# Optimization experiments

Hardware: AMD Instinct MI355X
Metric: run time of the kernel (lower is better)

Reference implementation:

```python
import jax, jax.numpy as jnp
import numpy as np

C = 256
HEADS = 8
HD = C // HEADS
EPS = 1e-5


def _layernorm(x, g, b):
    mu = jnp.mean(x, axis=-1, keepdims=True)
    var = jnp.var(x, axis=-1, keepdims=True)
    return (x - mu) * jax.lax.rsqrt(var + EPS) * g + b


def setup_inputs() -> dict:
    key = jax.random.key(0)
    ks = jax.random.split(key, 16)
    s = 0.02
    return {
        "x": jax.random.normal(ks[0], (1, C, 64, 64), jnp.float32),
        "bn_gamma": 1.0 + s * jax.random.normal(ks[1], (C,), jnp.float32),
        "bn_beta": s * jax.random.normal(ks[2], (C,), jnp.float32),
        "bn_mean": s * jax.random.normal(ks[3], (C,), jnp.float32),
        "bn_var": jnp.ones((C,), jnp.float32),
        "w_in": s * jax.random.normal(ks[4], (C, C), jnp.float32),
        "b_in": jnp.zeros((C,), jnp.float32),
        "ln1_g": jnp.ones((C,), jnp.float32),
        "ln1_b": jnp.zeros((C,), jnp.float32),
        "w_qkv": s * jax.random.normal(ks[5], (3 * C, C), jnp.float32),
        "b_qkv": jnp.zeros((3 * C,), jnp.float32),
        "w_ap": s * jax.random.normal(ks[6], (C, C), jnp.float32),
        "b_ap": jnp.zeros((C,), jnp.float32),
        "ln2_g": jnp.ones((C,), jnp.float32),
        "ln2_b": jnp.zeros((C,), jnp.float32),
        "w_ff1": s * jax.random.normal(ks[7], (4 * C, C), jnp.float32),
        "b_ff1": jnp.zeros((4 * C,), jnp.float32),
        "w_ff2": s * jax.random.normal(ks[8], (C, 4 * C), jnp.float32),
        "b_ff2": jnp.zeros((C,), jnp.float32),
        "w_out": s * jax.random.normal(ks[9], (C, C), jnp.float32),
        "b_out": jnp.zeros((C,), jnp.float32),
    }


def reference(x, bn_gamma, bn_beta, bn_mean, bn_var, w_in, b_in,
              ln1_g, ln1_b, w_qkv, b_qkv, w_ap, b_ap,
              ln2_g, ln2_b, w_ff1, b_ff1, w_ff2, b_ff2, w_out, b_out):
    b, c, h, w = x.shape
    t = h * w
    x_in = x
    # BatchNorm2d (eval mode: running stats)
    xn = (x - bn_mean[None, :, None, None]) * jax.lax.rsqrt(bn_var + EPS)[None, :, None, None]
    xn = xn * bn_gamma[None, :, None, None] + bn_beta[None, :, None, None]
    # proj_in 1x1 conv -> tokens [b, t, c]
    tok = xn.reshape(b, c, t).transpose(0, 2, 1)
    tok = tok @ w_in.T + b_in
    # transformer block (depth=1)
    y = _layernorm(tok, ln1_g, ln1_b)  # norm1
    qkv = y @ w_qkv.T + b_qkv  # [b, t, 3c], channel split (3, H, hd)
    qkv = qkv.reshape(b, t, 3, HEADS, HD)
    q = qkv[:, :, 0].transpose(0, 2, 1, 3)  # [b, H, t, hd]
    k = qkv[:, :, 1].transpose(0, 2, 1, 3)
    v = qkv[:, :, 2].transpose(0, 2, 1, 3)
    scale = HD ** (-0.5)
    attn = jax.nn.softmax(jnp.einsum('bhqd,bhkd->bhqk', q, k) * scale, axis=-1)
    o = jnp.einsum('bhqk,bhkd->bhqd', attn, v)  # [b, H, t, hd]
    o = o.transpose(0, 2, 1, 3).reshape(b, t, c)  # channels ordered (H, hd)
    o = o @ w_ap.T + b_ap  # attn proj 1x1
    attn_out = o + y  # VanillaAttention residual adds its (normed) input
    tok = tok + attn_out
    # FFN
    z = _layernorm(tok, ln2_g, ln2_b)
    z = jax.nn.gelu(z @ w_ff1.T + b_ff1, approximate=False)
    tok = tok + (z @ w_ff2.T + b_ff2)
    # back to image, proj_out 1x1, outer residual
    x4 = tok.transpose(0, 2, 1).reshape(b, c, h, w)
    out = jnp.einsum('oc,bchw->bohw', w_out, x4) + b_out[None, :, None, None]
    return out + x_in
```

## Files before the change

kernel.cpp:

```cpp
#include <hip/hip_runtime.h>
#include <math.h>

#define T_TOK 4096
#define C_DIM 256
#define EPSF  1e-5f
#define SC_QL (0.17677669529663687f * 1.4426950408889634f)

typedef short  bf16x8  __attribute__((ext_vector_type(8)));
typedef float  f32x4   __attribute__((ext_vector_type(4)));
typedef ushort ushort8 __attribute__((ext_vector_type(8)));
typedef unsigned uint4v __attribute__((ext_vector_type(4)));

__device__ __forceinline__ short f2bf(float f) {
    unsigned u = __builtin_bit_cast(unsigned, f);
    unsigned r = (u + 0x7FFFu + ((u >> 16) & 1u)) >> 16;
    return (short)r;
}
__device__ __forceinline__ float bf2f(ushort u) {
    return __builtin_bit_cast(float, ((unsigned)u) << 16);
}
__device__ __forceinline__ unsigned pk_bf16(float a, float b) {
    const unsigned ua = __builtin_bit_cast(unsigned, a) + 0x8000u;
    const unsigned ub = __builtin_bit_cast(unsigned, b) + 0x8000u;
    return __builtin_amdgcn_perm(ub, ua, 0x07060302u);
}
__device__ __forceinline__ unsigned cvtpk_bf16(float a, float b) {
    unsigned r;
    asm("v_cvt_pk_bf16_f32 %0, %1, %2" : "=v"(r) : "v"(a), "v"(b));
    return r;
}
__device__ __forceinline__ void plswap32(unsigned &a, unsigned &b) {
    asm("v_permlane32_swap_b32 %0, %1" : "+v"(a), "+v"(b));
}
__device__ __forceinline__ void plswap16(unsigned &a, unsigned &b) {
    asm("v_permlane16_swap_b32 %0, %1" : "+v"(a), "+v"(b));
}
template <int CTRL>
__device__ __forceinline__ float dppf(float x) {
    return __builtin_bit_cast(float,
        __builtin_amdgcn_mov_dpp(__builtin_bit_cast(int, x), CTRL, 0xF, 0xF, true));
}
__device__ __forceinline__ float rowsum16(float x) {
    x += dppf<0xB1>(x);
    x += dppf<0x4E>(x);
    x += dppf<0x141>(x);
    x += dppf<0x140>(x);
    return x;
}
#define MFMA16(a, b, c) __builtin_amdgcn_mfma_f32_16x16x32_bf16(a, b, c, 0, 0, 0)

__global__ __launch_bounds__(256) void prep_kernel(
    const float* __restrict__ w_in, const float* __restrict__ w_qkv,
    const float* __restrict__ w_ap, const float* __restrict__ w_ff1,
    const float* __restrict__ w_ff2, const float* __restrict__ w_out,
    const float* __restrict__ b_qkv, ushort* __restrict__ wbuf,
    float* __restrict__ bqs,
    const float* __restrict__ x, const float* __restrict__ gamma,
    const float* __restrict__ beta, const float* __restrict__ mean,
    const float* __restrict__ var, ushort* __restrict__ tin)
{
    __shared__ float tile[32][33];
    if (blockIdx.x < 896) {
        const int gid = blockIdx.x * 256 + threadIdx.x;
        const int e0 = gid * 4;
        const float* src; int off; float sc = 1.f;
        if (e0 < 65536)       { src = w_in;  off = e0; }
        else if (e0 < 262144) { src = w_qkv; off = e0 - 65536; if (off < 65536) sc = SC_QL; }
        else if (e0 < 327680) { src = w_ap;  off = e0 - 262144; }
        else if (e0 < 589824) { src = w_ff1; off = e0 - 327680; }
        else if (e0 < 851968) { src = w_ff2; off = e0 - 589824; }
        else                  { src = w_out; off = e0 - 851968; }
        const float4 v = *(const float4*)(src + off);
        ushort4 o;
        o.x = (ushort)f2bf(v.x * sc); o.y = (ushort)f2bf(v.y * sc);
        o.z = (ushort)f2bf(v.z * sc); o.w = (ushort)f2bf(v.w * sc);
        *(ushort4*)(wbuf + e0) = o;
        if (gid < 192) {
            const float s2 = (gid < 64) ? SC_QL : 1.f;
            float4 b = ((const float4*)b_qkv)[gid];
            b.x *= s2; b.y *= s2; b.z *= s2; b.w *= s2;
            ((float4*)bqs)[gid] = b;
        }
    } else {
        const int bidx = blockIdx.x - 896;
        const int t0 = (bidx & 127) * 32, c0 = (bidx >> 7) * 32;
        const int tx = threadIdx.x & 31, ty = threadIdx.x >> 5;
#pragma unroll
        for (int i = 0; i < 32; i += 8) {
            const int c = c0 + ty + i;
            const float a = rsqrtf(var[c] + EPSF) * gamma[c];
            const float d = beta[c] - mean[c] * a;
            tile[ty + i][tx] = x[c * T_TOK + t0 + tx] * a + d;
        }
        __syncthreads();
#pragma unroll
        for (int i = 0; i < 32; i += 8) {
            const int t = t0 + ty + i;
            tin[t * C_DIM + c0 + tx] = (ushort)f2bf(tile[tx][ty + i]);
        }
    }
}

__global__ __launch_bounds__(1024) void fused_pre(
    const ushort* __restrict__ tin, const ushort* __restrict__ wb_in,
    const float* __restrict__ b_in, const float* __restrict__ ln1_g,
    const float* __restrict__ ln1_b, const ushort* __restrict__ wb_qkv,
    const float* __restrict__ bqs, float* __restrict__ tok0,
    float* __restrict__ yout, ushort* __restrict__ qkvb)
{
    __shared__ ushort Atile[16 * 264];
    __shared__ ushort Ytile[16 * 264];
    __shared__ float  red[16][16][2];
    const int t0 = blockIdx.x * 16;
    const int tid = threadIdx.x, wv = tid >> 6, lane = tid & 63;
    const int c = lane & 15, g = lane >> 4;

    {
        const int r = tid >> 6, c0 = (tid & 63) * 4;
        *(ushort4*)&Atile[r * 264 + c0] = *(const ushort4*)(tin + (size_t)(t0 + r) * 256 + c0);
    }
    __syncthreads();

    f32x4 accp = {};
#pragma unroll
    for (int kc = 0; kc < 8; ++kc) {
        const bf16x8 af = *(const bf16x8*)&Atile[c * 264 + kc * 32 + g * 8];
        const bf16x8 bfv = *(const bf16x8*)(wb_in +
            (size_t)(wv * 16 + c) * 256 + kc * 32 + g * 8);
        accp = MFMA16(af, bfv, accp);
    }
    const int colp = wv * 16 + c;
    {
        const float bb = b_in[colp];
        float vs[4], s1[4], s2[4];
#pragma unroll
        for (int rr = 0; rr < 4; ++rr) {
            const float v = accp[rr] + bb;
            vs[rr] = v; s1[rr] = v; s2[rr] = v * v;
            tok0[(size_t)(t0 + 4 * g + rr) * 256 + colp] = v;
        }
#pragma unroll
        for (int rr = 0; rr < 4; ++rr) { s1[rr] = rowsum16(s1[rr]); s2[rr] = rowsum16(s2[rr]); }
        if (c == 0) {
#pragma unroll
            for (int rr = 0; rr < 4; ++rr) {
                red[wv][4 * g + rr][0] = s1[rr];
                red[wv][4 * g + rr][1] = s2[rr];
            }
        }
        __syncthreads();
        if (tid < 32) {
            const int row = tid >> 1, j = tid & 1;
            float s = 0.f;
#pragma unroll
            for (int w = 0; w < 16; ++w) s += red[w][row][j];
            red[0][row][j] = s;
        }
        __syncthreads();
        const float gg = ln1_g[colp], lb = ln1_b[colp];
#pragma unroll
        for (int rr = 0; rr < 4; ++rr) {
            const int row = 4 * g + rr;
            const float mu = red[0][row][0] * (1.0f / 256.0f);
            const float var = red[0][row][1] * (1.0f / 256.0f) - mu * mu;
            const float rs = rsqrtf(var + EPSF);
            const float yv = (vs[rr] - mu) * rs * gg + lb;
            yout[(size_t)(t0 + row) * 256 + colp] = yv;
            Ytile[row * 264 + colp] = (ushort)f2bf(yv);
        }
    }
    __syncthreads();

    f32x4 accq[3] = {};
#pragma unroll
    for (int kc = 0; kc < 8; ++kc) {
        const bf16x8 af = *(const bf16x8*)&Ytile[c * 264 + kc * 32 + g * 8];
#pragma unroll
        for (int nf = 0; nf < 3; ++nf) {
            const bf16x8 bfv = *(const bf16x8*)(wb_qkv +
                (size_t)(wv * 48 + nf * 16 + c) * 256 + kc * 32 + g * 8);
            accq[nf] = MFMA16(af, bfv, accq[nf]);
        }
    }
#pragma unroll
    for (int nf = 0; nf < 3; ++nf) {
        const int col = wv * 48 + nf * 16 + c;
        const float bb = bqs[col];
#pragma unroll
        for (int rr = 0; rr < 4; ++rr)
            qkvb[(size_t)(t0 + 4 * g + rr) * 768 + col] = (ushort)f2bf(accq[nf][rr] + bb);
    }
}

#define KS   40
#define VTS  72

__global__ __launch_bounds__(256) void attn_mfma(
    const ushort* __restrict__ qkv, ushort* __restrict__ o1,
    ushort* __restrict__ o2, ushort* __restrict__ o3,
    ushort* __restrict__ o4, float* __restrict__ lpart)
{
    const int h    = blockIdx.y;
    const int q0   = blockIdx.x << 6;
    const int qrt  = blockIdx.z;
    const int tid  = threadIdx.x;
    const int wv   = tid >> 6, lane = tid & 63;
    const int c    = lane & 15, g = lane >> 4;

    __shared__ ushort Ks[2][64 * KS];
    __shared__ ushort Vt[2][32 * VTS];

    const bf16x8 qf = *(const bf16x8*)(qkv + (size_t)(q0 + wv * 16 + c) * 768 + h * 32 + g * 8);

    bf16x8 ones;
#pragma unroll
    for (int i = 0; i < 8; ++i) ones[i] = (short)0x3F80;

    f32x4 oacc0 = {0.f, 0.f, 0.f, 0.f};
    f32x4 oacc1 = {0.f, 0.f, 0.f, 0.f};
    f32x4 oaccl = {0.f, 0.f, 0.f, 0.f};

    const int kr = tid >> 2, kc = (tid & 3) * 8;
    const int vp = tid & 31, vd = (tid >> 5) * 4;
    const ushort* kbase = qkv + 256 + h * 32;
    const ushort* vbase = qkv + 512 + h * 32;

    const int kt0 = qrt * 16, kt1 = kt0 + 16;

    {
        const ushort8 kv  = *(const ushort8*)(kbase + ((size_t)kt0 * 64 + kr) * 768 + kc);
        const ushort4 va = *(const ushort4*)(vbase + ((size_t)kt0 * 64 + 2 * vp) * 768 + vd);
        const ushort4 vb = *(const ushort4*)(vbase + ((size_t)kt0 * 64 + 2 * vp + 1) * 768 + vd);
        *(ushort8*)&Ks[0][kr * KS + kc] = kv;
        unsigned* vtp = (unsigned*)&Vt[0][0];
        vtp[(vd + 0) * (VTS / 2) + vp] = (unsigned)va.x | ((unsigned)vb.x << 16);
        vtp[(vd + 1) * (VTS / 2) + vp] = (unsigned)va.y | ((unsigned)vb.y << 16);
        vtp[(vd + 2) * (VTS / 2) + vp] = (unsigned)va.z | ((unsigned)vb.z << 16);
        vtp[(vd + 3) * (VTS / 2) + vp] = (unsigned)va.w | ((unsigned)vb.w << 16);
    }
    ushort8 kpre  = *(const ushort8*)(kbase + ((size_t)(kt0 + 1) * 64 + kr) * 768 + kc);
    ushort4 vpre0 = *(const ushort4*)(vbase + ((size_t)(kt0 + 1) * 64 + 2 * vp) * 768 + vd);
    ushort4 vpre1 = *(const ushort4*)(vbase + ((size_t)(kt0 + 1) * 64 + 2 * vp + 1) * 768 + vd);
    __syncthreads();

    int p = 0;
    for (int kt = kt0; kt < kt1; ++kt) {
        const ushort* ks = &Ks[p][0];
        const ushort* vt = &Vt[p][0];
        const bf16x8 k0 = *(const bf16x8*)&ks[(0 * 16 + c) * KS + g * 8];
        const bf16x8 k1 = *(const bf16x8*)&ks[(1 * 16 + c) * KS + g * 8];
        const bf16x8 k2 = *(const bf16x8*)&ks[(2 * 16 + c) * KS + g * 8];
        const bf16x8 k3 = *(const bf16x8*)&ks[(3 * 16 + c) * KS + g * 8];

        if (kt + 1 < kt1) {
            *(ushort8*)&Ks[p ^ 1][kr * KS + kc] = kpre;
            unsigned* vtp = (unsigned*)&Vt[p ^ 1][0];
            vtp[(vd + 0) * (VTS / 2) + vp] = (unsigned)vpre0.x | ((unsigned)vpre1.x << 16);
            vtp[(vd + 1) * (VTS / 2) + vp] = (unsigned)vpre0.y | ((unsigned)vpre1.y << 16);
            vtp[(vd + 2) * (VTS / 2) + vp] = (unsigned)vpre0.z | ((unsigned)vpre1.z << 16);
            vtp[(vd + 3) * (VTS / 2) + vp] = (unsigned)vpre0.w | ((unsigned)vpre1.w << 16);
            if (kt + 2 < kt1) {
                const size_t t2 = (size_t)(kt + 2) * 64;
                kpre  = *(const ushort8*)(kbase + (t2 + kr) * 768 + kc);
                vpre0 = *(const ushort4*)(vbase + (t2 + 2 * vp) * 768 + vd);
                vpre1 = *(const ushort4*)(vbase + (t2 + 2 * vp + 1) * 768 + vd);
            }
        }

        const f32x4 zz = {0.f, 0.f, 0.f, 0.f};
        const f32x4 s0 = MFMA16(k0, qf, zz);
        const f32x4 s1 = MFMA16(k1, qf, zz);
        const f32x4 s2 = MFMA16(k2, qf, zz);
        const f32x4 s3 = MFMA16(k3, qf, zz);

        unsigned w00 = cvtpk_bf16(__builtin_amdgcn_exp2f(s0[0]), __builtin_amdgcn_exp2f(s0[1]));
        unsigned w01 = cvtpk_bf16(__builtin_amdgcn_exp2f(s0[2]), __builtin_amdgcn_exp2f(s0[3]));
        unsigned w10 = cvtpk_bf16(__builtin_amdgcn_exp2f(s1[0]), __builtin_amdgcn_exp2f(s1[1]));
        unsigned w11 = cvtpk_bf16(__builtin_amdgcn_exp2f(s1[2]), __builtin_amdgcn_exp2f(s1[3]));
        unsigned w20 = cvtpk_bf16(__builtin_amdgcn_exp2f(s2[0]), __builtin_amdgcn_exp2f(s2[1]));
        unsigned w21 = cvtpk_bf16(__builtin_amdgcn_exp2f(s2[2]), __builtin_amdgcn_exp2f(s2[3]));
        unsigned w30 = cvtpk_bf16(__builtin_amdgcn_exp2f(s3[0]), __builtin_amdgcn_exp2f(s3[1]));
        unsigned w31 = cvtpk_bf16(__builtin_amdgcn_exp2f(s3[2]), __builtin_amdgcn_exp2f(s3[3]));

        plswap32(w00, w10); plswap16(w00, w10);
        plswap32(w01, w11); plswap16(w01, w11);
        plswap32(w20, w30); plswap16(w20, w30);
        plswap32(w21, w31); plswap16(w21, w31);
        const uint4v u0 = {w00, w01, w10, w11};
        const uint4v u1 = {w20, w21, w30, w31};
        const bf16x8 pa0 = __builtin_bit_cast(bf16x8, u0);
        const bf16x8 pa1 = __builtin_bit_cast(bf16x8, u1);

        {
            const bf16x8 va0 = *(const bf16x8*)&vt[(c)      * VTS + 0 * 32 + g * 8];
            const bf16x8 vb0 = *(const bf16x8*)&vt[(16 + c) * VTS + 0 * 32 + g * 8];
            oacc0 = MFMA16(pa0, va0, oacc0);
            oacc1 = MFMA16(pa0, vb0, oacc1);
            oaccl = MFMA16(pa0, ones, oaccl);
            const bf16x8 va1 = *(const bf16x8*)&vt[(c)      * VTS + 1 * 32 + g * 8];
            const bf16x8 vb1 = *(const bf16x8*)&vt[(16 + c) * VTS + 1 * 32 + g * 8];
            oacc0 = MFMA16(pa1, va1, oacc0);
            oacc1 = MFMA16(pa1, vb1, oacc1);
            oaccl = MFMA16(pa1, ones, oaccl);
        }
        p ^= 1;
        __syncthreads();
    }

    {
        ushort* ob = (qrt & 2) ? ((qrt & 1) ? o4 : o3) : ((qrt & 1) ? o2 : o1);
        ushort* op = ob + (size_t)(q0 + wv * 16) * 256 + h * 32;
#pragma unroll
        for (int rr = 0; rr < 4; ++rr) {
            op[(4 * g + rr) * 256 + c]      = (ushort)f2bf(oacc0[rr]);
            op[(4 * g + rr) * 256 + 16 + c] = (ushort)f2bf(oacc1[rr]);
        }
        if (c == 0) {
#pragma unroll
            for (int rr = 0; rr < 4; ++rr)
                lpart[(size_t)(q0 + wv * 16 + 4 * g + rr) * 32 + qrt * 8 + h] = oaccl[rr];
        }
    }
}

__global__ __launch_bounds__(1024) void fused_mid(
    const ushort* __restrict__ o1, const ushort* __restrict__ o2,
    const ushort* __restrict__ o3, const ushort* __restrict__ o4,
    const float* __restrict__ lpart, const ushort* __restrict__ wb_ap,
    const float* __restrict__ b_ap, const float* __restrict__ yin,
    const float* __restrict__ tok0, const float* __restrict__ ln2_g,
    const float* __restrict__ ln2_b, const ushort* __restrict__ wb_ff1,
    const float* __restrict__ b_ff1, float* __restrict__ tok1,
    ushort* __restrict__ zbuf)
{
    __shared__ ushort Otile[16 * 264];
    __shared__ ushort Ztile[16 * 264];
    __shared__ float  red[16][16][2];
    const int t0 = blockIdx.x * 16;
    const int tid = threadIdx.x, wv = tid >> 6, lane = tid & 63;
    const int c = lane & 15, g = lane >> 4;

    {
        const int r = tid >> 6, c0 = (tid & 63) * 4;
        const int h = (tid & 63) >> 3;
        const float* lp = lpart + (size_t)(t0 + r) * 32;
        const float inv = 1.0f / (lp[h] + lp[8 + h] + lp[16 + h] + lp[24 + h]);
        const size_t idx = (size_t)(t0 + r) * 256 + c0;
        const ushort4 a = *(const ushort4*)(o1 + idx);
        const ushort4 b = *(const ushort4*)(o2 + idx);
        const ushort4 d = *(const ushort4*)(o3 + idx);
        const ushort4 e = *(const ushort4*)(o4 + idx);
        unsigned w[2];
        w[0] = pk_bf16((bf2f(a.x) + bf2f(b.x) + bf2f(d.x) + bf2f(e.x)) * inv,
                       (bf2f(a.y) + bf2f(b.y) + bf2f(d.y) + bf2f(e.y)) * inv);
        w[1] = pk_bf16((bf2f(a.z) + bf2f(b.z) + bf2f(d.z) + bf2f(e.z)) * inv,
                       (bf2f(a.w) + bf2f(b.w) + bf2f(d.w) + bf2f(e.w)) * inv);
        *(ushort4*)&Otile[r * 264 + c0] = *(ushort4*)w;
    }
    __syncthreads();

    f32x4 accp = {};
#pragma unroll
    for (int kc = 0; kc < 8; ++kc) {
        const bf16x8 af = *(const bf16x8*)&Otile[c * 264 + kc * 32 + g * 8];
        const bf16x8 bfv = *(const bf16x8*)(wb_ap +
            (size_t)(wv * 16 + c) * 256 + kc * 32 + g * 8);
        accp = MFMA16(af, bfv, accp);
    }
    const int colp = wv * 16 + c;
    {
        const float bb = b_ap[colp];
        float vs[4], s1[4], s2[4];
#pragma unroll
        for (int rr = 0; rr < 4; ++rr) {
            const size_t idx = (size_t)(t0 + 4 * g + rr) * 256 + colp;
            const float v = accp[rr] + bb + yin[idx] + tok0[idx];
            vs[rr] = v; s1[rr] = v; s2[rr] = v * v;
            tok1[idx] = v;
        }
#pragma unroll
        for (int rr = 0; rr < 4; ++rr) { s1[rr] = rowsum16(s1[rr]); s2[rr] = rowsum16(s2[rr]); }
        if (c == 0) {
#pragma unroll
            for (int rr = 0; rr < 4; ++rr) {
                red[wv][4 * g + rr][0] = s1[rr];
                red[wv][4 * g + rr][1] = s2[rr];
            }
        }
        __syncthreads();
        if (tid < 32) {
            const int row = tid >> 1, j = tid & 1;
            float s = 0.f;
#pragma unroll
            for (int w = 0; w < 16; ++w) s += red[w][row][j];
            red[0][row][j] = s;
        }
        __syncthreads();
        const float gg = ln2_g[colp], lb = ln2_b[colp];
#pragma unroll
        for (int rr = 0; rr < 4; ++rr) {
            const int row = 4 * g + rr;
            const float mu = red[0][row][0] * (1.0f / 256.0f);
            const float var = red[0][row][1] * (1.0f / 256.0f) - mu * mu;
            const float rs = rsqrtf(var + EPSF);
            const float zv = (vs[rr] - mu) * rs * gg + lb;
            Ztile[row * 264 + colp] = (ushort)f2bf(zv);
        }
    }
    __syncthreads();

    f32x4 accf[4] = {};
#pragma unroll
    for (int kc = 0; kc < 8; ++kc) {
        const bf16x8 af = *(const bf16x8*)&Ztile[c * 264 + kc * 32 + g * 8];
#pragma unroll
        for (int nf = 0; nf < 4; ++nf) {
            const bf16x8 bfv = *(const bf16x8*)(wb_ff1 +
                (size_t)(wv * 64 + nf * 16 + c) * 256 + kc * 32 + g * 8);
            accf[nf] = MFMA16(af, bfv, accf[nf]);
        }
    }
#pragma unroll
    for (int nf = 0; nf < 4; ++nf) {
        const int col = wv * 64 + nf * 16 + c;
        const float bb = b_ff1[col];
#pragma unroll
        for (int rr = 0; rr < 4; ++rr) {
            float v = accf[nf][rr] + bb;
            v = 0.5f * v * (1.0f + erff(v * 0.70710678118654752f));
            zbuf[(size_t)(t0 + 4 * g + rr) * 1024 + col] = (ushort)f2bf(v);
        }
    }
}

__global__ __launch_bounds__(1024) void fused_post(
    const ushort* __restrict__ zbuf, const ushort* __restrict__ wb_ff2,
    const float* __restrict__ b_ff2, const float* __restrict__ tok1,
    const ushort* __restrict__ wb_out, const float* __restrict__ b_out,
    const float* __restrict__ x, float* __restrict__ out)
{
    __shared__ ushort Ztile[16 * 1032];
    __shared__ ushort T2tile[16 * 264];
    const int t0 = blockIdx.x * 16;
    const int tid = threadIdx.x, wv = tid >> 6, lane = tid & 63;
    const int c = lane & 15, g = lane >> 4;

    {
        const int r = tid >> 6, c0 = (tid & 63) * 16;
        *(ushort8*)&Ztile[r * 1032 + c0] =
            *(const ushort8*)(zbuf + (size_t)(t0 + r) * 1024 + c0);
        *(ushort8*)&Ztile[r * 1032 + c0 + 8] =
            *(const ushort8*)(zbuf + (size_t)(t0 + r) * 1024 + c0 + 8);
    }
    __syncthreads();

    f32x4 accf = {};
#pragma unroll
    for (int kc = 0; kc < 32; ++kc) {
        const bf16x8 af = *(const bf16x8*)&Ztile[c * 1032 + kc * 32 + g * 8];
        const bf16x8 bfv = *(const bf16x8*)(wb_ff2 +
            (size_t)(wv * 16 + c) * 1024 + kc * 32 + g * 8);
        accf = MFMA16(af, bfv, accf);
    }
    {
        const int col = wv * 16 + c;
        const float bb = b_ff2[col];
#pragma unroll
        for (int rr = 0; rr < 4; ++rr) {
            const size_t idx = (size_t)(t0 + 4 * g + rr) * 256 + col;
            const float v = accf[rr] + bb + tok1[idx];
            T2tile[(4 * g + rr) * 264 + col] = (ushort)f2bf(v);
        }
    }
    __syncthreads();

    f32x4 acco = {};
#pragma unroll
    for (int kc = 0; kc < 8; ++kc) {
        const bf16x8 bfr = *(const bf16x8*)&T2tile[c * 264 + kc * 32 + g * 8];
        const bf16x8 afr = *(const bf16x8*)(wb_out +
            (size_t)(wv * 16 + c) * 256 + kc * 32 + g * 8);
        acco = MFMA16(afr, bfr, acco);
    }
#pragma unroll
    for (int rr = 0; rr < 4; ++rr) {
        const int och = wv * 16 + 4 * g + rr;
        const size_t idx = (size_t)och * T_TOK + t0 + c;
        out[idx] = acco[rr] + b_out[och] + x[idx];
    }
}

extern "C" void kernel_launch(void* const* d_in, const int* in_sizes, int n_in,
                              void* d_out, int out_size, void* d_ws, size_t ws_size,
                              hipStream_t stream)
{
    const float* x     = (const float*)d_in[0];
    const float* bn_g  = (const float*)d_in[1];
    const float* bn_b  = (const float*)d_in[2];
    const float* bn_m  = (const float*)d_in[3];
    const float* bn_v  = (const float*)d_in[4];
    const float* w_in  = (const float*)d_in[5];
    const float* b_in  = (const float*)d_in[6];
    const float* ln1_g = (const float*)d_in[7];
    const float* ln1_b = (const float*)d_in[8];
    const float* w_qkv = (const float*)d_in[9];
    const float* b_qkv = (const float*)d_in[10];
    const float* w_ap  = (const float*)d_in[11];
    const float* b_ap  = (const float*)d_in[12];
    const float* ln2_g = (const float*)d_in[13];
    const float* ln2_b = (const float*)d_in[14];
    const float* w_ff1 = (const float*)d_in[15];
    const float* b_ff1 = (const float*)d_in[16];
    const float* w_ff2 = (const float*)d_in[17];
    const float* b_ff2 = (const float*)d_in[18];
    const float* w_out = (const float*)d_in[19];
    const float* b_out = (const float*)d_in[20];
    float* out = (float*)d_out;
    float* ws  = (float*)d_ws;

    const size_t MF = 1u << 20;
    float*  tok0   = ws;
    float*  y      = ws + MF;
    float*  tok1   = ws + 2 * MF;
    ushort* qkv_bf = (ushort*)(ws + 3 * MF);
    ushort* zbuf   = (ushort*)(ws + 4 * MF + MF / 2);
    ushort* tin_bf = (ushort*)(ws + 6 * MF + MF / 2);
    ushort* o1p    = tin_bf;
    ushort* o2p    = (ushort*)(ws + 7 * MF);
    ushort* o3p    = (ushort*)(ws + 7 * MF + MF / 2);
    ushort* o4p    = (ushort*)(ws + 8 * MF);
    float*  lpart  = ws + 8 * MF + MF / 2;
    ushort* wbuf   = (ushort*)(ws + 8 * MF + MF / 2 + 131072);
    const ushort* wb_in  = wbuf;
    const ushort* wb_qkv = wbuf + 65536;
    const ushort* wb_ap  = wbuf + 262144;
    const ushort* wb_ff1 = wbuf + 327680;
    const ushort* wb_ff2 = wbuf + 589824;
    const ushort* wb_out = wbuf + 851968;
    float* bqs = (float*)(wbuf + 917504);

    prep_kernel<<<1920, 256, 0, stream>>>(w_in, w_qkv, w_ap, w_ff1, w_ff2, w_out,
                                          b_qkv, wbuf, bqs,
                                          x, bn_g, bn_b, bn_m, bn_v, tin_bf);
    fused_pre<<<256, 1024, 0, stream>>>(tin_bf, wb_in, b_in, ln1_g, ln1_b,
                                        wb_qkv, bqs, tok0, y, qkv_bf);
    attn_mfma<<<dim3(64, 8, 4), 256, 0, stream>>>(qkv_bf, o1p, o2p, o3p, o4p, lpart);
    fused_mid<<<256, 1024, 0, stream>>>(o1p, o2p, o3p, o4p, lpart, wb_ap, b_ap,
                                        y, tok0, ln2_g, ln2_b, wb_ff1, b_ff1,
                                        tok1, zbuf);
    fused_post<<<256, 1024, 0, stream>>>(zbuf, wb_ff2, b_ff2, tok1, wb_out, b_out,
                                         x, out);
}
```

Measured before the change: 203.0 us.

## Split attention launch by head halves and retune K/V staging loads

The attention kernel launch is split into two launches of four heads each, using a new head-offset argument. The K tile load mapping now follows the wave/lane fragment layout instead of a flat thread index. V loads become 32-bit-pair vector loads whose halves are interleaved with byte-permute instructions rather than shift-or packing. The aim is cheaper V transposition into shared memory and possibly better cache locality per launch, at the cost of an extra kernel launch and a serialization point between the halves.

Result: slower. 214.2 us (+5.5%).

```diff
diff --git a/kernel.cpp b/kernel.cpp
--- a/kernel.cpp
+++ b/kernel.cpp
@@ -10,6 +10,7 @@
 typedef float  f32x4   __attribute__((ext_vector_type(4)));
 typedef ushort ushort8 __attribute__((ext_vector_type(8)));
 typedef unsigned uint4v __attribute__((ext_vector_type(4)));
+typedef unsigned uint2v __attribute__((ext_vector_type(2)));
 
 __device__ __forceinline__ short f2bf(float f) {
     unsigned u = __builtin_bit_cast(unsigned, f);
@@ -198,9 +199,9 @@
 __global__ __launch_bounds__(256) void attn_mfma(
     const ushort* __restrict__ qkv, ushort* __restrict__ o1,
     ushort* __restrict__ o2, ushort* __restrict__ o3,
-    ushort* __restrict__ o4, float* __restrict__ lpart)
+    ushort* __restrict__ o4, float* __restrict__ lpart, int h0)
 {
-    const int h    = blockIdx.y;
+    const int h    = h0 + blockIdx.y;
     const int q0   = blockIdx.x << 6;
     const int qrt  = blockIdx.z;
     const int tid  = threadIdx.x;
@@ -220,7 +221,7 @@
     f32x4 oacc1 = {0.f, 0.f, 0.f, 0.f};
     f32x4 oaccl = {0.f, 0.f, 0.f, 0.f};
 
-    const int kr = tid >> 2, kc = (tid & 3) * 8;
+    const int kr = wv * 16 + c, kc = g * 8;
     const int vp = tid & 31, vd = (tid >> 5) * 4;
     const ushort* kbase = qkv + 256 + h * 32;
     const ushort* vbase = qkv + 512 + h * 32;
@@ -228,19 +229,19 @@
     const int kt0 = qrt * 16, kt1 = kt0 + 16;
 
     {
-        const ushort8 kv  = *(const ushort8*)(kbase + ((size_t)kt0 * 64 + kr) * 768 + kc);
-        const ushort4 va = *(const ushort4*)(vbase + ((size_t)kt0 * 64 + 2 * vp) * 768 + vd);
-        const ushort4 vb = *(const ushort4*)(vbase + ((size_t)kt0 * 64 + 2 * vp + 1) * 768 + vd);
+        const ushort8 kv = *(const ushort8*)(kbase + ((size_t)kt0 * 64 + kr) * 768 + kc);
+        const uint2v va = *(const uint2v*)(vbase + ((size_t)kt0 * 64 + 2 * vp) * 768 + vd);
+        const uint2v vb = *(const uint2v*)(vbase + ((size_t)kt0 * 64 + 2 * vp + 1) * 768 + vd);
         *(ushort8*)&Ks[0][kr * KS + kc] = kv;
         unsigned* vtp = (unsigned*)&Vt[0][0];
-        vtp[(vd + 0) * (VTS / 2) + vp] = (unsigned)va.x | ((unsigned)vb.x << 16);
-        vtp[(vd + 1) * (VTS / 2) + vp] = (unsigned)va.y | ((unsigned)vb.y << 16);
-        vtp[(vd + 2) * (VTS / 2) + vp] = (unsigned)va.z | ((unsigned)vb.z << 16);
-        vtp[(vd + 3) * (VTS / 2) + vp] = (unsigned)va.w | ((unsigned)vb.w << 16);
-    }
-    ushort8 kpre  = *(const ushort8*)(kbase + ((size_t)(kt0 + 1) * 64 + kr) * 768 + kc);
-    ushort4 vpre0 = *(const ushort4*)(vbase + ((size_t)(kt0 + 1) * 64 + 2 * vp) * 768 + vd);
-    ushort4 vpre1 = *(const ushort4*)(vbase + ((size_t)(kt0 + 1) * 64 + 2 * vp + 1) * 768 + vd);
+        vtp[(vd + 0) * (VTS / 2) + vp] = __builtin_amdgcn_perm(vb.x, va.x, 0x05040100u);
+        vtp[(vd + 1) * (VTS / 2) + vp] = __builtin_amdgcn_perm(vb.x, va.x, 0x07060302u);
+        vtp[(vd + 2) * (VTS / 2) + vp] = __builtin_amdgcn_perm(vb.y, va.y, 0x05040100u);
+        vtp[(vd + 3) * (VTS / 2) + vp] = __builtin_amdgcn_perm(vb.y, va.y, 0x07060302u);
+    }
+    ushort8 kpre = *(const ushort8*)(kbase + ((size_t)(kt0 + 1) * 64 + kr) * 768 + kc);
+    uint2v vpre0 = *(const uint2v*)(vbase + ((size_t)(kt0 + 1) * 64 + 2 * vp) * 768 + vd);
+    uint2v vpre1 = *(const uint2v*)(vbase + ((size_t)(kt0 + 1) * 64 + 2 * vp + 1) * 768 + vd);
     __syncthreads();
 
     int p = 0;
@@ -255,15 +256,15 @@
         if (kt + 1 < kt1) {
             *(ushort8*)&Ks[p ^ 1][kr * KS + kc] = kpre;
             unsigned* vtp = (unsigned*)&Vt[p ^ 1][0];
-            vtp[(vd + 0) * (VTS / 2) + vp] = (unsigned)vpre0.x | ((unsigned)vpre1.x << 16);
-            vtp[(vd + 1) * (VTS / 2) + vp] = (unsigned)vpre0.y | ((unsigned)vpre1.y << 16);
-            vtp[(vd + 2) * (VTS / 2) + vp] = (unsigned)vpre0.z | ((unsigned)vpre1.z << 16);
-            vtp[(vd + 3) * (VTS / 2) + vp] = (unsigned)vpre0.w | ((unsigned)vpre1.w << 16);
+            vtp[(vd + 0) * (VTS / 2) + vp] = __builtin_amdgcn_perm(vpre1.x, vpre0.x, 0x05040100u);
+            vtp[(vd + 1) * (VTS / 2) + vp] = __builtin_amdgcn_perm(vpre1.x, vpre0.x, 0x07060302u);
+            vtp[(vd + 2) * (VTS / 2) + vp] = __builtin_amdgcn_perm(vpre1.y, vpre0.y, 0x05040100u);
+            vtp[(vd + 3) * (VTS / 2) + vp] = __builtin_amdgcn_perm(vpre1.y, vpre0.y, 0x07060302u);
             if (kt + 2 < kt1) {
                 const size_t t2 = (size_t)(kt + 2) * 64;
                 kpre  = *(const ushort8*)(kbase + (t2 + kr) * 768 + kc);
-                vpre0 = *(const ushort4*)(vbase + (t2 + 2 * vp) * 768 + vd);
-                vpre1 = *(const ushort4*)(vbase + (t2 + 2 * vp + 1) * 768 + vd);
+                vpre0 = *(const uint2v*)(vbase + (t2 + 2 * vp) * 768 + vd);
+                vpre1 = *(const uint2v*)(vbase + (t2 + 2 * vp + 1) * 768 + vd);
             }
         }
 
@@ -544,7 +545,8 @@
                                           x, bn_g, bn_b, bn_m, bn_v, tin_bf);
     fused_pre<<<256, 1024, 0, stream>>>(tin_bf, wb_in, b_in, ln1_g, ln1_b,
                                         wb_qkv, bqs, tok0, y, qkv_bf);
-    attn_mfma<<<dim3(64, 8, 4), 256, 0, stream>>>(qkv_bf, o1p, o2p, o3p, o4p, lpart);
+    attn_mfma<<<dim3(64, 4, 4), 256, 0, stream>>>(qkv_bf, o1p, o2p, o3p, o4p, lpart, 0);
+    attn_mfma<<<dim3(64, 4, 4), 256, 0, stream>>>(qkv_bf, o1p, o2p, o3p, o4p, lpart, 4);
     fused_mid<<<256, 1024, 0, stream>>>(o1p, o2p, o3p, o4p, lpart, wb_ap, b_ap,
                                         y, tok0, ln2_g, ln2_b, wb_ff1, b_ff1,
                                         tok1, zbuf);
```
